# Performance work log

Measured on AMD Instinct MI355X. Metric: run time of the kernel, lower is better.

The kernel has to match this reference:

```python
import jax, jax.numpy as jnp
import numpy as np

N_NODES = 100000
N_EDGES = 1250000
IN_DIM = 6
HID = 64


def gcn_conv(x, W, b, src, dst, deg_inv_sqrt):
    # x: [N, F_in] -> [N, F_out]; symmetric-normalized aggregation with self-loops
    h = x @ W  # [N, F_out]
    norm = deg_inv_sqrt[src] * deg_inv_sqrt[dst]  # [E]
    msg = h[src] * norm[:, None]                  # gather + scale, [E, F_out]
    agg = jax.ops.segment_sum(msg, dst, num_segments=x.shape[0])
    # self-loop contribution: norm = deg_inv_sqrt[i]^2 = 1/deg[i]
    out = agg + h * (deg_inv_sqrt ** 2)[:, None] + b
    return out


def setup_inputs() -> dict:
    key = jax.random.key(0)
    ks = jax.random.split(key, 8)
    x = jax.random.normal(ks[0], (N_NODES, IN_DIM), dtype=jnp.float32)
    edge_index = jax.random.randint(ks[1], (2, N_EDGES), 0, N_NODES, dtype=jnp.int64)
    s1 = 1.0 / np.sqrt(IN_DIM)
    s2 = 1.0 / np.sqrt(HID)
    W1 = jax.random.uniform(ks[2], (IN_DIM, HID), jnp.float32, -s1, s1)
    b1 = jnp.zeros((HID,), jnp.float32)
    W2 = jax.random.uniform(ks[3], (HID, HID), jnp.float32, -s2, s2)
    b2 = jnp.zeros((HID,), jnp.float32)
    Wfc = jax.random.uniform(ks[4], (HID, 1), jnp.float32, -s2, s2)
    bfc = jnp.zeros((1,), jnp.float32)
    return {"x": x, "edge_index": edge_index, "W1": W1, "b1": b1,
            "W2": W2, "b2": b2, "Wfc": Wfc, "bfc": bfc}


def reference(x, edge_index, W1, b1, W2, b2, Wfc, bfc):
    src, dst = edge_index[0], edge_index[1]
    n = x.shape[0]
    # degree with self-loops (GCN default): in-degree at destination + 1
    deg = jax.ops.segment_sum(jnp.ones((src.shape[0],), x.dtype), dst, num_segments=n) + 1.0
    deg_inv_sqrt = jax.lax.rsqrt(deg)
    h = gcn_conv(x, W1, b1, src, dst, deg_inv_sqrt)
    h = jax.nn.relu(h)
    h = gcn_conv(h, W2, b2, src, dst, deg_inv_sqrt)
    g = h.mean(axis=0)              # [HID] graph readout
    out = jax.nn.sigmoid(g @ Wfc + bfc)  # [1]
    return out
```

## Files before the change

### kernel.cpp

```cpp
#include <hip/hip_runtime.h>
#include <math.h>

#define N_NODES 100000
#define N_EDGES 1250000
#define IN_DIM 6
#define HID 64

#define BIN_SHIFT 8
#define BIN_NODES 256
#define NBIN 391
#define A_BLOCKS 250
#define EPB (N_EDGES / A_BLOCKS)
#define CAP 4096
#define SOFF (NBIN * CAP)

__device__ inline float lo16(unsigned u) { return __uint_as_float(u << 16); }
__device__ inline float hi16(unsigned u) { return __uint_as_float(u & 0xffff0000u); }
__device__ inline unsigned short f2bf(float f) {
    unsigned u = __float_as_uint(f);
    u += 0x7FFFu + ((u >> 16) & 1u);
    return (unsigned short)(u >> 16);
}
__device__ inline unsigned pack2(float a, float b) {
    return (unsigned)f2bf(a) | ((unsigned)f2bf(b) << 16);
}

__global__ __launch_bounds__(1024) void binFill(const int* __restrict__ src,
                                                const int* __restrict__ dst,
                                                int* __restrict__ cnt,
                                                unsigned* __restrict__ rec) {
    __shared__ int lc[NBIN];
    __shared__ int scv[NBIN];
    __shared__ int lb[NBIN];
    __shared__ int lbase[NBIN];
    __shared__ unsigned ldsRec[EPB];
    __shared__ int ldsPos[EPB];

    int t = threadIdx.x;
    int base = blockIdx.x * EPB;

    int4 dA = *(const int4*)&dst[base + t * 4];
    int4 sA = *(const int4*)&src[base + t * 4];
    const int TB = (EPB - 4096) / 4;
    bool hasB = (t < TB);
    int4 dB = make_int4(0, 0, 0, 0), sB = make_int4(0, 0, 0, 0);
    if (hasB) {
        dB = *(const int4*)&dst[base + 4096 + t * 4];
        sB = *(const int4*)&src[base + 4096 + t * 4];
    }

#define HIST4(v4) do {                                  \
        atomicAdd(&lc[(v4).x >> BIN_SHIFT], 1);         \
        atomicAdd(&lc[(v4).y >> BIN_SHIFT], 1);         \
        atomicAdd(&lc[(v4).z >> BIN_SHIFT], 1);         \
        atomicAdd(&lc[(v4).w >> BIN_SHIFT], 1);         \
    } while (0)

#define SCAT1(key, val) do {                                                  \
        int b_ = (key) >> BIN_SHIFT;                                          \
        int loc_ = lbase[b_] + atomicAdd(&lc[b_], 1);                         \
        loc_ = min(loc_, EPB - 1);                                            \
        ldsRec[loc_] = ((unsigned)((key) & (BIN_NODES - 1)) << 17)            \
                     | (unsigned)(val);                                       \
        ldsPos[loc_] = lb[b_] + (loc_ - lbase[b_]);                           \
    } while (0)

#define SCAT4(k4, v4) do {                  \
        SCAT1((k4).x, (v4).x);              \
        SCAT1((k4).y, (v4).y);              \
        SCAT1((k4).z, (v4).z);              \
        SCAT1((k4).w, (v4).w);              \
    } while (0)

#define WRITEOUT() do {                                                       \
        for (int i = t; i < EPB; i += 1024) {                                 \
            unsigned p_ = (unsigned)ldsPos[i];                                \
            if (p_ < (unsigned)(2 * SOFF)) rec[p_] = ldsRec[i];               \
        }                                                                     \
    } while (0)

    if (t < NBIN) lc[t] = 0;
    __syncthreads();
    HIST4(dA);
    if (hasB) HIST4(dB);
    __syncthreads();
    if (t < NBIN) {
        int c = lc[t];
        scv[t] = c;
        lc[t] = 0;
        int off = (c > 0) ? atomicAdd(&cnt[t], c) : 0;
        lb[t] = t * CAP + off;
    }
    __syncthreads();
    if (t < 64) {
        int carry = 0;
#pragma unroll
        for (int cb = 0; cb < NBIN; cb += 64) {
            int idx = cb + t;
            int c = (idx < NBIN) ? scv[idx] : 0;
            int v = c;
#pragma unroll
            for (int off = 1; off < 64; off <<= 1) {
                int u = __shfl_up(v, off, 64);
                if (t >= off) v += u;
            }
            if (idx < NBIN) lbase[idx] = carry + v - c;
            carry += __shfl(v, 63, 64);
        }
    }
    __syncthreads();
    SCAT4(dA, sA);
    if (hasB) SCAT4(dB, sB);
    __syncthreads();
    WRITEOUT();
    __syncthreads();

    if (t < NBIN) lc[t] = 0;
    __syncthreads();
    HIST4(sA);
    if (hasB) HIST4(sB);
    __syncthreads();
    if (t < NBIN) {
        int c = lc[t];
        scv[t] = c;
        lc[t] = 0;
        int off = (c > 0) ? atomicAdd(&cnt[NBIN + t], c) : 0;
        lb[t] = SOFF + t * CAP + off;
    }
    __syncthreads();
    if (t < 64) {
        int carry = 0;
#pragma unroll
        for (int cb = 0; cb < NBIN; cb += 64) {
            int idx = cb + t;
            int c = (idx < NBIN) ? scv[idx] : 0;
            int v = c;
#pragma unroll
            for (int off = 1; off < 64; off <<= 1) {
                int u = __shfl_up(v, off, 64);
                if (t >= off) v += u;
            }
            if (idx < NBIN) lbase[idx] = carry + v - c;
            carry += __shfl(v, 63, 64);
        }
    }
    __syncthreads();
    SCAT4(sA, dA);
    if (hasB) SCAT4(sB, dB);
    __syncthreads();
    WRITEOUT();

#undef HIST4
#undef SCAT1
#undef SCAT4
#undef WRITEOUT
}

__global__ __launch_bounds__(1024) void disXH(const unsigned* __restrict__ rec,
                                              const int* __restrict__ cnt,
                                              const float* __restrict__ x,
                                              int* __restrict__ deg,
                                              float* __restrict__ dis,
                                              uint4* __restrict__ xpad) {
    __shared__ int histS[4][BIN_NODES];
    int t = threadIdx.x, g = t >> 8;
    if (t < 4 * BIN_NODES) ((int*)histS)[t] = 0;
    __syncthreads();
    int bin = blockIdx.x;
    int beg = bin * CAP, end = beg + cnt[bin];
    for (int j = beg + t; j < end; j += 1024) atomicAdd(&histS[g][rec[j] >> 17], 1);
    __syncthreads();
    if (t < BIN_NODES) {
        int n = (bin << BIN_SHIFT) + t;
        if (n < N_NODES) {
            int h = histS[0][t] + histS[1][t] + histS[2][t] + histS[3][t];
            deg[n] = h;
            float d = rsqrtf((float)h + 1.0f);
            dis[n] = d;
            float2 xa = *(const float2*)&x[n * IN_DIM + 0];
            float2 xb = *(const float2*)&x[n * IN_DIM + 2];
            float2 xc = *(const float2*)&x[n * IN_DIM + 4];
            uint4 u;
            u.x = pack2(xa.x * d, xa.y * d);
            u.y = pack2(xb.x * d, xb.y * d);
            u.z = pack2(xc.x * d, xc.y * d);
            u.w = 0;
            xpad[n] = u;
        }
    }
}

__global__ __launch_bounds__(1024) void aggW(const unsigned* __restrict__ rec,
                                             const int* __restrict__ cnt,
                                             const int* __restrict__ deg,
                                             const float* __restrict__ dis,
                                             const uint4* __restrict__ xpad,
                                             const float* __restrict__ W1,
                                             const float* __restrict__ b1,
                                             float* __restrict__ vsum) {
    __shared__ unsigned srcL[CAP];
    __shared__ float wlS[4][BIN_NODES];
    __shared__ int degL[BIN_NODES];
    __shared__ int startS[BIN_NODES];
    __shared__ int cur[BIN_NODES];
    __shared__ int sc[BIN_NODES];
    __shared__ float sAll[BIN_NODES][8];
    __shared__ float w1s[IN_DIM * HID];
    __shared__ float b1s[HID];
    __shared__ float vpart[HID];
    int t = threadIdx.x, g = t >> 8;
    int bin = blockIdx.x;

    if (t < 4 * BIN_NODES) ((float*)wlS)[t] = 0.f;
    if (t < IN_DIM * HID) w1s[t] = W1[t];
    if (t >= 1024 - HID) { int c = t - (1024 - HID); b1s[c] = b1[c]; vpart[c] = 0.f; }
    __syncthreads();

    {
        int beg = SOFF + bin * CAP, end = beg + cnt[NBIN + bin];
        for (int j = beg + t; j < end; j += 1024) {
            unsigned r = rec[j];
            atomicAdd(&wlS[g][r >> 17], dis[r & 131071u]);
        }
    }
    __syncthreads();

    if (t < BIN_NODES) {
        int n = (bin << BIN_SHIFT) + t;
        int h = (n < N_NODES) ? deg[n] : 0;
        degL[t] = h;
        sc[t] = h;
        float d = (n < N_NODES) ? rsqrtf((float)h + 1.0f) : 0.f;
        float wloc = wlS[0][t] + wlS[1][t] + wlS[2][t] + wlS[3][t];
        sAll[t][6] = d;
        sAll[t][7] = (n < N_NODES) ? d * (wloc + d) : 0.f;
    }
    __syncthreads();
    for (int off = 1; off < BIN_NODES; off <<= 1) {
        int add = 0;
        if (t < BIN_NODES && t >= off) add = sc[t - off];
        __syncthreads();
        if (t < BIN_NODES) sc[t] += add;
        __syncthreads();
    }
    if (t < BIN_NODES) {
        int st = sc[t] - degL[t];
        startS[t] = st;
        cur[t] = st;
    }
    __syncthreads();

    {
        int beg = bin * CAP, end = beg + cnt[bin];
        for (int j = beg + t; j < end; j += 1024) {
            unsigned r = rec[j];
            int pos = atomicAdd(&cur[r >> 17], 1);
            if (pos < CAP) srcL[pos] = r & 131071u;
        }
    }
    __syncthreads();

    {
        int node = t >> 2, sub = t & 3;
        int st = startS[node], cn = degL[node];
        int lim = min(st + cn, CAP);
        float s0 = 0.f, s1 = 0.f, s2 = 0.f, s3 = 0.f, s4 = 0.f, s5 = 0.f;
        for (int k = st + sub; k < lim; k += 4) {
            uint4 px = xpad[srcL[k]];
            s0 += lo16(px.x); s1 += hi16(px.x);
            s2 += lo16(px.y); s3 += hi16(px.y);
            s4 += lo16(px.z); s5 += hi16(px.z);
        }
        s0 += __shfl_xor(s0, 1, 64); s0 += __shfl_xor(s0, 2, 64);
        s1 += __shfl_xor(s1, 1, 64); s1 += __shfl_xor(s1, 2, 64);
        s2 += __shfl_xor(s2, 1, 64); s2 += __shfl_xor(s2, 2, 64);
        s3 += __shfl_xor(s3, 1, 64); s3 += __shfl_xor(s3, 2, 64);
        s4 += __shfl_xor(s4, 1, 64); s4 += __shfl_xor(s4, 2, 64);
        s5 += __shfl_xor(s5, 1, 64); s5 += __shfl_xor(s5, 2, 64);
        if (sub == 0) {
            int n = (bin << BIN_SHIFT) + node;
            if (n < N_NODES) {
                uint4 px = xpad[n];
                s0 += lo16(px.x); s1 += hi16(px.x);
                s2 += lo16(px.y); s3 += hi16(px.y);
                s4 += lo16(px.z); s5 += hi16(px.z);
            }
            sAll[node][0] = s0; sAll[node][1] = s1; sAll[node][2] = s2;
            sAll[node][3] = s3; sAll[node][4] = s4; sAll[node][5] = s5;
        }
    }
    __syncthreads();

    {
        int c = t & 63, grp = t >> 6;
        float v = 0.f;
#pragma unroll
        for (int i = 0; i < 16; ++i) {
            int node = grp * 16 + i;
            float d = sAll[node][6], cw = sAll[node][7];
            float a = sAll[node][0] * w1s[0 * HID + c]
                    + sAll[node][1] * w1s[1 * HID + c]
                    + sAll[node][2] * w1s[2 * HID + c]
                    + sAll[node][3] * w1s[3 * HID + c]
                    + sAll[node][4] * w1s[4 * HID + c]
                    + sAll[node][5] * w1s[5 * HID + c];
            v += cw * fmaxf(d * a + b1s[c], 0.f);
        }
        atomicAdd(&vpart[c], v);
    }
    __syncthreads();
    if (t < HID) atomicAdd(&vsum[t], vpart[t]);
}

__global__ void finalK(const float* __restrict__ vsum, const float* __restrict__ W2,
                       const float* __restrict__ b2, const float* __restrict__ Wfc,
                       const float* __restrict__ bfc, float* __restrict__ out) {
    __shared__ float vL[HID];
    int t = threadIdx.x;
    vL[t] = vsum[t] * (1.0f / N_NODES);
    __syncthreads();
    float g = b2[t];
    for (int k = 0; k < HID; ++k) g += vL[k] * W2[k * HID + t];
    float z = g * Wfc[t];
    for (int off = 32; off > 0; off >>= 1) z += __shfl_down(z, off, 64);
    if (t == 0) out[0] = 1.0f / (1.0f + expf(-(z + bfc[0])));
}

extern "C" void kernel_launch(void* const* d_in, const int* in_sizes, int n_in,
                              void* d_out, int out_size, void* d_ws, size_t ws_size,
                              hipStream_t stream) {
    const float* x   = (const float*)d_in[0];
    const int*   ei  = (const int*)d_in[1];
    const float* W1  = (const float*)d_in[2];
    const float* b1  = (const float*)d_in[3];
    const float* W2  = (const float*)d_in[4];
    const float* b2  = (const float*)d_in[5];
    const float* Wfc = (const float*)d_in[6];
    const float* bfc = (const float*)d_in[7];
    const int* src = ei;
    const int* dst = ei + N_EDGES;

    char* ws = (char*)d_ws;
    size_t off = 0;
    auto alloc = (+[](char* base, size_t* o, size_t bytes) {
        char* p = base + *o;
        *o += (bytes + 255) & ~(size_t)255;
        return p;
    });
    int*      cnt  = (int*)     alloc(ws, &off, (size_t)2 * NBIN * 4);
    float*    vsum = (float*)   alloc(ws, &off, 64 * 4);
    uint4*    xpad = (uint4*)   alloc(ws, &off, (size_t)N_NODES * 16);
    float*    dis  = (float*)   alloc(ws, &off, (size_t)N_NODES * 4);
    int*      deg  = (int*)     alloc(ws, &off, (size_t)N_NODES * 4);
    unsigned* rec  = (unsigned*)alloc(ws, &off, (size_t)2 * SOFF * 4);

    hipMemsetAsync(cnt, 0, ((size_t)2 * NBIN * 4 + 255 & ~(size_t)255) + 64 * 4, stream);

    binFill<<<A_BLOCKS, 1024, 0, stream>>>(src, dst, cnt, rec);
    disXH<<<NBIN, 1024, 0, stream>>>(rec, cnt, x, deg, dis, xpad);
    aggW<<<NBIN, 1024, 0, stream>>>(rec, cnt, deg, dis, xpad, W1, b1, vsum);
    finalK<<<1, 64, 0, stream>>>(vsum, W2, b2, Wfc, bfc, (float*)d_out);
}
```

Measured before the change: 124.0 us.

## Fuse final readout into aggregation kernel via last-block counter and wave-scan prefix

Removes the separate finalK launch by having the last block of aggW, detected with an atomic done counter and threadfence, compute the W2/Wfc readout and sigmoid. The 256-entry prefix sum over bin degrees becomes a single-wave shuffle scan, replacing a shared-memory Hillis-Steele loop that needed many block-wide barriers. The workspace layout is reordered so one memset clears the counters, vsum and the done flag together. The fused path adds a global atomic and a fence in every block.

```diff
diff --git a/kernel.cpp b/kernel.cpp
--- a/kernel.cpp
+++ b/kernel.cpp
@@ -197,17 +197,23 @@
                                              const uint4* __restrict__ xpad,
                                              const float* __restrict__ W1,
                                              const float* __restrict__ b1,
-                                             float* __restrict__ vsum) {
+                                             const float* __restrict__ W2,
+                                             const float* __restrict__ b2,
+                                             const float* __restrict__ Wfc,
+                                             const float* __restrict__ bfc,
+                                             float* __restrict__ vsum,
+                                             int* __restrict__ done,
+                                             float* __restrict__ out) {
     __shared__ unsigned srcL[CAP];
     __shared__ float wlS[4][BIN_NODES];
     __shared__ int degL[BIN_NODES];
     __shared__ int startS[BIN_NODES];
     __shared__ int cur[BIN_NODES];
-    __shared__ int sc[BIN_NODES];
     __shared__ float sAll[BIN_NODES][8];
     __shared__ float w1s[IN_DIM * HID];
     __shared__ float b1s[HID];
     __shared__ float vpart[HID];
+    __shared__ int lastFlag;
     int t = threadIdx.x, g = t >> 8;
     int bin = blockIdx.x;
 
@@ -229,24 +235,29 @@
         int n = (bin << BIN_SHIFT) + t;
         int h = (n < N_NODES) ? deg[n] : 0;
         degL[t] = h;
-        sc[t] = h;
         float d = (n < N_NODES) ? rsqrtf((float)h + 1.0f) : 0.f;
         float wloc = wlS[0][t] + wlS[1][t] + wlS[2][t] + wlS[3][t];
         sAll[t][6] = d;
         sAll[t][7] = (n < N_NODES) ? d * (wloc + d) : 0.f;
     }
     __syncthreads();
-    for (int off = 1; off < BIN_NODES; off <<= 1) {
-        int add = 0;
-        if (t < BIN_NODES && t >= off) add = sc[t - off];
-        __syncthreads();
-        if (t < BIN_NODES) sc[t] += add;
-        __syncthreads();
-    }
-    if (t < BIN_NODES) {
-        int st = sc[t] - degL[t];
-        startS[t] = st;
-        cur[t] = st;
+    if (t < 64) {
+        int carry = 0;
+#pragma unroll
+        for (int cb = 0; cb < BIN_NODES; cb += 64) {
+            int idx = cb + t;
+            int c = degL[idx];
+            int v = c;
+#pragma unroll
+            for (int off = 1; off < 64; off <<= 1) {
+                int u = __shfl_up(v, off, 64);
+                if (t >= off) v += u;
+            }
+            int st = carry + v - c;
+            startS[idx] = st;
+            cur[idx] = st;
+            carry += __shfl(v, 63, 64);
+        }
     }
     __syncthreads();
 
@@ -310,20 +321,23 @@
     }
     __syncthreads();
     if (t < HID) atomicAdd(&vsum[t], vpart[t]);
-}
-
-__global__ void finalK(const float* __restrict__ vsum, const float* __restrict__ W2,
-                       const float* __restrict__ b2, const float* __restrict__ Wfc,
-                       const float* __restrict__ bfc, float* __restrict__ out) {
-    __shared__ float vL[HID];
-    int t = threadIdx.x;
-    vL[t] = vsum[t] * (1.0f / N_NODES);
-    __syncthreads();
-    float g = b2[t];
-    for (int k = 0; k < HID; ++k) g += vL[k] * W2[k * HID + t];
-    float z = g * Wfc[t];
-    for (int off = 32; off > 0; off >>= 1) z += __shfl_down(z, off, 64);
-    if (t == 0) out[0] = 1.0f / (1.0f + expf(-(z + bfc[0])));
+    __syncthreads();
+
+    if (t == 0) {
+        __threadfence();
+        lastFlag = (atomicAdd(done, 1) == NBIN - 1);
+    }
+    __syncthreads();
+    if (lastFlag && t < 64) {
+        float vv = atomicAdd(&vsum[t], 0.0f) * (1.0f / N_NODES);
+        float gacc = b2[t];
+#pragma unroll 8
+        for (int k = 0; k < HID; ++k)
+            gacc += __shfl(vv, k, 64) * W2[k * HID + t];
+        float z = gacc * Wfc[t];
+        for (int off = 32; off > 0; off >>= 1) z += __shfl_down(z, off, 64);
+        if (t == 0) out[0] = 1.0f / (1.0f + expf(-(z + bfc[0])));
+    }
 }
 
 extern "C" void kernel_launch(void* const* d_in, const int* in_sizes, int n_in,
@@ -349,15 +363,16 @@
     });
     int*      cnt  = (int*)     alloc(ws, &off, (size_t)2 * NBIN * 4);
     float*    vsum = (float*)   alloc(ws, &off, 64 * 4);
+    int*      done = (int*)     alloc(ws, &off, 4);
+    int*      deg  = (int*)     alloc(ws, &off, (size_t)N_NODES * 4);
+    float*    dis  = (float*)   alloc(ws, &off, (size_t)N_NODES * 4);
     uint4*    xpad = (uint4*)   alloc(ws, &off, (size_t)N_NODES * 16);
-    float*    dis  = (float*)   alloc(ws, &off, (size_t)N_NODES * 4);
-    int*      deg  = (int*)     alloc(ws, &off, (size_t)N_NODES * 4);
     unsigned* rec  = (unsigned*)alloc(ws, &off, (size_t)2 * SOFF * 4);
 
-    hipMemsetAsync(cnt, 0, ((size_t)2 * NBIN * 4 + 255 & ~(size_t)255) + 64 * 4, stream);
+    hipMemsetAsync(cnt, 0, (size_t)((char*)deg - (char*)cnt), stream);
 
     binFill<<<A_BLOCKS, 1024, 0, stream>>>(src, dst, cnt, rec);
     disXH<<<NBIN, 1024, 0, stream>>>(rec, cnt, x, deg, dis, xpad);
-    aggW<<<NBIN, 1024, 0, stream>>>(rec, cnt, deg, dis, xpad, W1, b1, vsum);
-    finalK<<<1, 64, 0, stream>>>(vsum, W2, b2, Wfc, bfc, (float*)d_out);
-}
+    aggW<<<NBIN, 1024, 0, stream>>>(rec, cnt, deg, dis, xpad, W1, b1,
+                                    W2, b2, Wfc, bfc, vsum, done, (float*)d_out);
+}
```

New measurement: 128.4 us. +3.6%, slower.
